# Performance work log

Hardware: AMD Instinct MI355X
Metric: run time of the kernel (lower is better)

## Reference

```python
import math
import jax, jax.numpy as jnp
import numpy as np

NUM_HEADS = 16
LN_EPS = 1e-5


def setup_inputs() -> dict:
    key = jax.random.key(0)
    ks = jax.random.split(key, 8)
    B, S, D = 2, 1024, 1024
    L, H = 4, NUM_HEADS
    hd = D // H
    return {
        "x": jax.random.normal(ks[0], (B, S, D), jnp.float32),
        "past_k": jax.random.normal(ks[1], (L, B, H, S, hd), jnp.float32),
        "past_v": jax.random.normal(ks[2], (L, B, H, S, hd), jnp.float32),
        "past_q": jax.random.normal(ks[3], (L, B, H, S, hd), jnp.float32),
        "Wqkv": jax.random.normal(ks[4], (3 * D, D), jnp.float32) * 0.02,
        "bqkv": jnp.zeros((3 * D,), jnp.float32),
        "Wout": jax.random.normal(ks[5], (D, D), jnp.float32) * 0.02,
        "bout": jnp.zeros((D,), jnp.float32),
    }


def reference(x, past_k, past_v, past_q, Wqkv, bqkv, Wout, bout):
    B, S, D = x.shape
    H = NUM_HEADS
    hd = D // H
    scale = 1.0 / math.sqrt(hd)

    # qkv projection + head split: [B,S,D] -> [B,H,S,hd] each
    qkv = x @ Wqkv.T + bqkv  # [B,S,3D]
    q, k, v = jnp.split(qkv, 3, axis=-1)
    split = lambda t: t.reshape(B, S, H, hd).transpose(0, 2, 1, 3)
    q, k, v = split(q), split(k), split(v)

    # causal token attention scores [B,H,S,S]
    token_scores = jnp.einsum("bhqd,bhkd->bhqk", q, k) * scale
    causal = jnp.triu(jnp.ones((S, S), bool), k=1)
    token_scores = jnp.where(causal, -jnp.inf, token_scores)

    # stack past layers: [L,B,H,S,hd] -> [B,S,L,D]
    def to_full(t):
        L = t.shape[0]
        return t.transpose(1, 3, 0, 2, 4).reshape(B, S, L, D)

    mem = jnp.concatenate([to_full(past_q), to_full(past_k), to_full(past_v)], axis=2)  # [B,S,M,D], M=3L
    M = mem.shape[2]

    # layer norm (no affine) over feature dim
    mu = mem.mean(-1, keepdims=True)
    var = mem.var(-1, keepdims=True)
    mem = (mem - mu) / jnp.sqrt(var + LN_EPS)

    # reproject through K/V slices of qkv weight
    Wk, bk = Wqkv[D:2 * D], bqkv[D:2 * D]
    Wv, bv = Wqkv[2 * D:], bqkv[2 * D:]
    rk = (mem @ Wk.T + bk).reshape(B, S, M, H, hd).transpose(0, 3, 1, 2, 4)  # [B,H,S,M,hd]
    rv = (mem @ Wv.T + bv).reshape(B, S, M, H, hd).transpose(0, 3, 1, 2, 4)

    # memory scores via per-position elementwise reduce [B,H,S,M]
    mem_scores = jnp.einsum("bhsd,bhsmd->bhsm", q, rk) * scale

    scores = jnp.concatenate([token_scores, mem_scores], axis=-1)  # [B,H,S,S+M]
    weights = jax.nn.softmax(scores, axis=-1)
    token_w, mem_w = weights[..., :S], weights[..., S:]

    token_ctx = jnp.einsum("bhqk,bhkd->bhqd", token_w, v)
    mem_ctx = jnp.einsum("bhsm,bhsmd->bhsd", mem_w, rv)
    attn = token_ctx + mem_ctx  # [B,H,S,hd]

    merged = attn.transpose(0, 2, 1, 3).reshape(B, S, D)
    out = merged @ Wout.T + bout
    return out, (k, v, q)
```

## Files before the change

kernel.cpp:

```cpp
#include <hip/hip_runtime.h>

#define BATCH 2
#define SEQ   1024
#define DIM   1024
#define NH    16
#define HD    64
#define NM    12
#define NTOK  (BATCH*SEQ)
#define MEMROWS (BATCH*SEQ*NM)
#define OUTT  2097152
#define NEGBIG (-1.0e30f)

typedef __attribute__((ext_vector_type(8))) short short8;
typedef __attribute__((ext_vector_type(4))) float f32x4;

__device__ __forceinline__ float bf2f(ushort u) {
    union { unsigned int i; float f; } t; t.i = ((unsigned int)u) << 16; return t.f;
}
__device__ __forceinline__ ushort f2bf(float f) {
    union { float f; unsigned int i; } t; t.f = f;
    unsigned int i = t.i;
    unsigned int lsb = (i >> 16) & 1u;
    i += 0x7fffu + lsb;
    return (ushort)(i >> 16);
}

__global__ __launch_bounds__(256) void cvt3_kernel(
    const float* __restrict__ a, ushort* __restrict__ ab, int na4,
    const float* __restrict__ b, ushort* __restrict__ bb, int nb4,
    const float* __restrict__ c, ushort* __restrict__ cb, int nc4)
{
    int i = blockIdx.x * 256 + threadIdx.x;
    if (i >= na4 + nb4 + nc4) return;
    const float* src; ushort* dst; int j;
    if (i < na4)            { src = a; dst = ab; j = i; }
    else if (i < na4 + nb4) { src = b; dst = bb; j = i - na4; }
    else                    { src = c; dst = cb; j = i - na4 - nb4; }
    float4 v = ((const float4*)src)[j];
    ushort4 o; o.x = f2bf(v.x); o.y = f2bf(v.y); o.z = f2bf(v.z); o.w = f2bf(v.w);
    ((ushort4*)dst)[j] = o;
}


#define QKV_BLKS 384
__global__ __launch_bounds__(256) void qkv_ln_fused_kernel(
    const ushort* __restrict__ xb, const ushort* __restrict__ Wb,
    const float* __restrict__ bias, float* __restrict__ out,
    ushort* __restrict__ qkvb,
    const float* __restrict__ pq, const float* __restrict__ pk,
    const float* __restrict__ pv, ushort* __restrict__ mem_n)
{
    const int bid = blockIdx.x;
    const int tid = threadIdx.x;
    if (bid < QKV_BLKS) {
        __shared__ ushort As[128][40];
        __shared__ ushort Bs[128][40];
        const int w = tid >> 6, lane = tid & 63;
        const int n = lane & 15, qd = lane >> 4;
        const int wr = (w >> 1) * 64, wc = (w & 1) * 64;
        const int row0 = (bid / 24) * 128, col0 = (bid % 24) * 128;
        const int r1 = tid >> 2, o1 = (tid & 3) * 8;
        const int r2 = (tid + 256) >> 2, o2 = ((tid + 256) & 3) * 8;

        f32x4 acc[4][4];
#pragma unroll
        for (int mt = 0; mt < 4; mt++)
#pragma unroll
            for (int nt = 0; nt < 4; nt++) acc[mt][nt] = (f32x4){0.f, 0.f, 0.f, 0.f};

        for (int k0 = 0; k0 < 1024; k0 += 32) {
            *(short8*)&As[r1][o1] = *(const short8*)(xb + (size_t)(row0 + r1) * 1024 + k0 + o1);
            *(short8*)&As[r2][o2] = *(const short8*)(xb + (size_t)(row0 + r2) * 1024 + k0 + o2);
            *(short8*)&Bs[r1][o1] = *(const short8*)(Wb + (size_t)(col0 + r1) * 1024 + k0 + o1);
            *(short8*)&Bs[r2][o2] = *(const short8*)(Wb + (size_t)(col0 + r2) * 1024 + k0 + o2);
            __syncthreads();
            short8 af[4], bf[4];
#pragma unroll
            for (int mt = 0; mt < 4; mt++) af[mt] = *(const short8*)&As[wr + mt * 16 + n][qd * 8];
#pragma unroll
            for (int nt = 0; nt < 4; nt++) bf[nt] = *(const short8*)&Bs[wc + nt * 16 + n][qd * 8];
#pragma unroll
            for (int mt = 0; mt < 4; mt++)
#pragma unroll
                for (int nt = 0; nt < 4; nt++)
                    acc[mt][nt] = __builtin_amdgcn_mfma_f32_16x16x32_bf16(af[mt], bf[nt], acc[mt][nt], 0, 0, 0);
            __syncthreads();
        }
#pragma unroll
        for (int mt = 0; mt < 4; mt++)
#pragma unroll
            for (int nt = 0; nt < 4; nt++)
#pragma unroll
                for (int r = 0; r < 4; r++) {
                    int row = row0 + wr + mt * 16 + qd * 4 + r;
                    int col = col0 + wc + nt * 16 + n;
                    float val = acc[mt][nt][r] + bias[col];
                    int t = col >> 10, h = (col >> 6) & 15, d = col & 63;
                    int b = row >> 10, s = row & 1023;
                    size_t idx = (((size_t)(b * NH + h) * SEQ + s) * HD) + d;
                    size_t base = (t == 0) ? (size_t)3 * OUTT : (t == 1) ? (size_t)OUTT : (size_t)2 * OUTT;
                    out[base + idx] = val;
                    qkvb[(size_t)t * OUTT + idx] = f2bf(val);
                }
    } else {
        const int wid = tid >> 6, lane = tid & 63;
        const int r = (bid - QKV_BLKS) * 4 + wid;
        const int idx = r % NM;
        const int bs = r / NM;
        const int s = bs & (SEQ - 1);
        const int b = bs >> 10;
        const int c = idx >> 2;
        const int l = idx & 3;
        const float* src = (c == 0) ? pq : ((c == 1) ? pk : pv);
        const size_t base = ((size_t)(l * BATCH + b) * NH) * (SEQ * HD) + (size_t)s * HD;

        float4 v4[4];
        float sum = 0.f, sumsq = 0.f;
#pragma unroll
        for (int p = 0; p < 4; p++) {
            int h = p * 4 + (lane >> 4);
            int d = (lane & 15) * 4;
            float4 v = *(const float4*)(src + base + (size_t)h * (SEQ * HD) + d);
            v4[p] = v;
            sum   += v.x + v.y + v.z + v.w;
            sumsq += v.x * v.x + v.y * v.y + v.z * v.z + v.w * v.w;
        }
#pragma unroll
        for (int off = 32; off > 0; off >>= 1) {
            sum   += __shfl_xor(sum, off);
            sumsq += __shfl_xor(sumsq, off);
        }
        float mu  = sum * (1.f / 1024.f);
        float var = fmaxf(sumsq * (1.f / 1024.f) - mu * mu, 0.f);
        float inv = rsqrtf(var + 1e-5f);
        ushort* dst = mem_n + (size_t)r * 1024;
#pragma unroll
        for (int p = 0; p < 4; p++) {
            int dp = (p * 64 + lane) * 4;
            ushort4 o;
            o.x = f2bf((v4[p].x - mu) * inv);
            o.y = f2bf((v4[p].y - mu) * inv);
            o.z = f2bf((v4[p].z - mu) * inv);
            o.w = f2bf((v4[p].w - mu) * inv);
            *(ushort4*)(dst + dp) = o;
        }
    }
}

__global__ __launch_bounds__(256) void mfma_out_kernel(
    const ushort* __restrict__ Ab, const ushort* __restrict__ Wb,
    const float* __restrict__ bias, float* __restrict__ C)
{
    __shared__ ushort As[128][40];
    __shared__ ushort Bs[128][40];
    const int tid = threadIdx.x;
    const int w = tid >> 6, lane = tid & 63;
    const int n = lane & 15, qd = lane >> 4;
    const int wr = (w >> 1) * 64, wc = (w & 1) * 64;
    const int row0 = blockIdx.y * 128, col0 = blockIdx.x * 128;
    const int r1 = tid >> 2, o1 = (tid & 3) * 8;
    const int r2 = (tid + 256) >> 2, o2 = ((tid + 256) & 3) * 8;

    f32x4 acc[4][4];
#pragma unroll
    for (int mt = 0; mt < 4; mt++)
#pragma unroll
        for (int nt = 0; nt < 4; nt++) acc[mt][nt] = (f32x4){0.f, 0.f, 0.f, 0.f};

    for (int k0 = 0; k0 < 1024; k0 += 32) {
        *(short8*)&As[r1][o1] = *(const short8*)(Ab + (size_t)(row0 + r1) * 1024 + k0 + o1);
        *(short8*)&As[r2][o2] = *(const short8*)(Ab + (size_t)(row0 + r2) * 1024 + k0 + o2);
        *(short8*)&Bs[r1][o1] = *(const short8*)(Wb + (size_t)(col0 + r1) * 1024 + k0 + o1);
        *(short8*)&Bs[r2][o2] = *(const short8*)(Wb + (size_t)(col0 + r2) * 1024 + k0 + o2);
        __syncthreads();
        short8 af[4], bf[4];
#pragma unroll
        for (int mt = 0; mt < 4; mt++) af[mt] = *(const short8*)&As[wr + mt * 16 + n][qd * 8];
#pragma unroll
        for (int nt = 0; nt < 4; nt++) bf[nt] = *(const short8*)&Bs[wc + nt * 16 + n][qd * 8];
#pragma unroll
        for (int mt = 0; mt < 4; mt++)
#pragma unroll
            for (int nt = 0; nt < 4; nt++)
                acc[mt][nt] = __builtin_amdgcn_mfma_f32_16x16x32_bf16(af[mt], bf[nt], acc[mt][nt], 0, 0, 0);
        __syncthreads();
    }
#pragma unroll
    for (int mt = 0; mt < 4; mt++)
#pragma unroll
        for (int nt = 0; nt < 4; nt++)
#pragma unroll
            for (int r = 0; r < 4; r++) {
                int row = row0 + wr + mt * 16 + qd * 4 + r;
                int col = col0 + wc + nt * 16 + n;
                C[(size_t)row * 1024 + col] = acc[mt][nt][r] + bias[col];
            }
}

__global__ __launch_bounds__(256) void mfma_vproj_kernel(
    const ushort* __restrict__ wvecb, const ushort* __restrict__ Wvb,
    const float* __restrict__ bv, const float* __restrict__ wmem,
    ushort* __restrict__ mergedb)
{
    __shared__ ushort As[128][40];
    __shared__ ushort Bs[64][40];
    const int tid = threadIdx.x;
    const int w = tid >> 6, lane = tid & 63;
    const int n = lane & 15, qd = lane >> 4;
    const int wr = (w >> 1) * 64, wc = (w & 1) * 32;
    const int row0 = blockIdx.x * 128;
    const int h = blockIdx.y;
    const int r1 = tid >> 2, o1 = (tid & 3) * 8;
    const int r2 = (tid + 256) >> 2, o2 = ((tid + 256) & 3) * 8;

    f32x4 acc[4][2];
#pragma unroll
    for (int mt = 0; mt < 4; mt++)
#pragma unroll
        for (int nt = 0; nt < 2; nt++) acc[mt][nt] = (f32x4){0.f, 0.f, 0.f, 0.f};

    for (int k0 = 0; k0 < 1024; k0 += 32) {
        *(short8*)&As[r1][o1] = *(const short8*)(wvecb + ((size_t)(row0 + r1) * NH + h) * 1024 + k0 + o1);
        *(short8*)&As[r2][o2] = *(const short8*)(wvecb + ((size_t)(row0 + r2) * NH + h) * 1024 + k0 + o2);
        *(short8*)&Bs[r1 & 63][o1] = *(const short8*)(Wvb + (size_t)(h * HD + (r1 & 63)) * 1024 + k0 + o1);
        __syncthreads();
        short8 af[4], bf[2];
#pragma unroll
        for (int mt = 0; mt < 4; mt++) af[mt] = *(const short8*)&As[wr + mt * 16 + n][qd * 8];
#pragma unroll
        for (int nt = 0; nt < 2; nt++) bf[nt] = *(const short8*)&Bs[wc + nt * 16 + n][qd * 8];
#pragma unroll
        for (int mt = 0; mt < 4; mt++)
#pragma unroll
            for (int nt = 0; nt < 2; nt++)
                acc[mt][nt] = __builtin_amdgcn_mfma_f32_16x16x32_bf16(af[mt], bf[nt], acc[mt][nt], 0, 0, 0);
        __syncthreads();
    }
#pragma unroll
    for (int mt = 0; mt < 4; mt++)
#pragma unroll
        for (int nt = 0; nt < 2; nt++)
#pragma unroll
            for (int r = 0; r < 4; r++) {
                int token = row0 + wr + mt * 16 + qd * 4 + r;
                int d = wc + nt * 16 + n;
                float ws = wmem[((size_t)token * NH + h) * 16 + 12];
                size_t mi = (size_t)token * DIM + h * HD + d;
                float val = bf2f(mergedb[mi]) + acc[mt][nt][r] + ws * bv[h * HD + d];
                mergedb[mi] = f2bf(val);
            }
}

#define MSC_T 8
__global__ __launch_bounds__(256) void msc_direct_kernel(
    const ushort* __restrict__ qkvb, const ushort* __restrict__ mem_n,
    const ushort* __restrict__ Wkb, const float* __restrict__ bqkv,
    float* __restrict__ msc0, float* __restrict__ msc1)
{
    __shared__ ushort wks[4][64][72];
    __shared__ ushort qpc[4][MSC_T][4][72];

    const int tid = threadIdx.x;
    const int w = tid >> 6, lane = tid & 63;
    const int n = lane & 15, qd = lane >> 4;
    const int t0 = blockIdx.x * MSC_T;
    const int kh = blockIdx.y;

    short8 af0[4], af1[4];
    {
        const int g = t0 + (n & 7), b = g >> 10, s = g & 1023;
#pragma unroll
        for (int hh = 0; hh < 4; hh++) {
            const int h = w * 4 + hh;
            const ushort* qrow = qkvb + (((size_t)(b * NH + h) * SEQ + s) * HD);
            af0[hh] = *(const short8*)(qrow + qd * 8);
            af1[hh] = *(const short8*)(qrow + 32 + qd * 8);
        }
    }
    float qbkv[4] = {0.f, 0.f, 0.f, 0.f};
    if (kh == 0) {
#pragma unroll
        for (int hh = 0; hh < 4; hh++) {
            const int h = w * 4 + hh;
            const float* bk = bqkv + DIM + h * HD;
            float s = 0.f;
#pragma unroll
            for (int j = 0; j < 8; j++) {
                s += bf2f((ushort)af0[hh][j]) * bk[qd * 8 + j];
                s += bf2f((ushort)af1[hh][j]) * bk[32 + qd * 8 + j];
            }
            s += __shfl_xor(s, 16);
            s += __shfl_xor(s, 32);
            qbkv[hh] = s;
        }
    }

    f32x4 acc[MSC_T];
#pragma unroll
    for (int t = 0; t < MSC_T; t++) acc[t] = (f32x4){0.f, 0.f, 0.f, 0.f};

    for (int ch = 0; ch < 8; ch++) {
        const int c0 = (kh * 8 + ch) * 64;
#pragma unroll
        for (int hh = 0; hh < 4; hh++) {
            const int h = w * 4 + hh;
            const ushort* wsrc = Wkb + (size_t)(h * HD + lane) * 1024 + c0;
#pragma unroll
            for (int j = 0; j < 4; j++) {
                ushort t16[16];
                *(short8*)&t16[0] = *(const short8*)(wsrc + j * 16);
                *(short8*)&t16[8] = *(const short8*)(wsrc + j * 16 + 8);
#pragma unroll
                for (int c = 0; c < 16; c++) wks[w][j * 16 + c][lane] = t16[c];
            }
#pragma unroll
            for (int nt = 0; nt < 4; nt++) {
                short8 bf0 = *(const short8*)&wks[w][nt * 16 + n][qd * 8];
                short8 bf1 = *(const short8*)&wks[w][nt * 16 + n][32 + qd * 8];
                f32x4 z = (f32x4){0.f, 0.f, 0.f, 0.f};
                z = __builtin_amdgcn_mfma_f32_16x16x32_bf16(af0[hh], bf0, z, 0, 0, 0);
                z = __builtin_amdgcn_mfma_f32_16x16x32_bf16(af1[hh], bf1, z, 0, 0, 0);
                if (qd < 2) {
#pragma unroll
                    for (int r = 0; r < 4; r++)
                        qpc[w][qd * 4 + r][hh][nt * 16 + n] = f2bf(z[r]);
                }
            }
        }
#pragma unroll
        for (int t = 0; t < MSC_T; t++) {
            const int g = t0 + t;
            const int mrow = (n < NM) ? n : 0;
            const ushort* mb = mem_n + ((size_t)g * NM + mrow) * 1024 + c0;
            short8 a0 = *(const short8*)&qpc[w][t][n & 3][qd * 8];
            short8 a1 = *(const short8*)&qpc[w][t][n & 3][32 + qd * 8];
            short8 b0 = *(const short8*)(mb + qd * 8);
            short8 b1 = *(const short8*)(mb + 32 + qd * 8);
            acc[t] = __builtin_amdgcn_mfma_f32_16x16x32_bf16(a0, b0, acc[t], 0, 0, 0);
            acc[t] = __builtin_amdgcn_mfma_f32_16x16x32_bf16(a1, b1, acc[t], 0, 0, 0);
        }
    }
#pragma unroll
    for (int t = 0; t < MSC_T; t++) {
        const size_t g = t0 + t;
#pragma unroll
        for (int r = 0; r < 4; r++) {
            float qb = __shfl(qbkv[r], t);
            if (qd == 0 && n < NM) {
                const int h = w * 4 + r;
                if (kh == 0)
                    msc0[(g * NH + h) * NM + n] = 0.125f * (acc[t][r] + qb);
                else
                    msc1[(g * NH + h) * NM + n] = 0.125f * acc[t][r];
            }
        }
    }
}

#define TQ 64
#define TK 64
__global__ __launch_bounds__(512) void flash_attn_kernel(
    const ushort* __restrict__ qkvb, const float* __restrict__ msc0,
    const float* __restrict__ msc1,
    ushort* __restrict__ mergedb, float* __restrict__ wmem)
{
    __shared__ __align__(16) char smem[55296];
    ushort (*Ks)[TK][72]  = (ushort (*)[TK][72])smem;
    ushort (*Vt)[HD][72]  = (ushort (*)[HD][72])(smem + 18432);
    ushort (*Ps)[16][72]  = (ushort (*)[16][72])(smem + 36864);
    float  (*cbuf)[64][25] = (float (*)[64][25])smem;

    const int bxr = blockIdx.x;
    const int qt = (bxr & 1) ? (bxr >> 1) : (15 - (bxr >> 1));
    const int bh = blockIdx.y;
    const int b = bh >> 4, h = bh & 15;
    const int tid = threadIdx.x;
    const int w = tid >> 6;
    const int g = w >> 2;
    const int wq = w & 3;
    const int lane = tid & 63;
    const int n = lane & 15;
    const int qd = lane >> 4;

    const ushort* qb = qkvb;
    const ushort* kb = qkvb + (size_t)OUTT;
    const ushort* vb = qkvb + (size_t)2 * OUTT;
    const size_t headoff = (size_t)bh * SEQ * HD;

    const int qrow0 = qt * TQ + wq * 16;
    const ushort* qp = qb + headoff + (size_t)(qrow0 + n) * HD;
    short8 qf0 = *(const short8*)(qp + qd * 8);
    short8 qf1 = *(const short8*)(qp + 32 + qd * 8);

    float mrow[4], lrow[4];
    f32x4 Oacc[4];
#pragma unroll
    for (int r = 0; r < 4; r++) { mrow[r] = NEGBIG; lrow[r] = 0.f; }
#pragma unroll
    for (int nt = 0; nt < 4; nt++) Oacc[nt] = (f32x4){0.f, 0.f, 0.f, 0.f};

    const int gtid = tid & 255;
    const int key = gtid >> 2;
    const int c0 = (gtid & 3) * 16;
    const int nsteps = (qt + 2) >> 1;

    for (int step = 0; step < nsteps; ++step) {
        const int kt = 2 * step + g;
        const bool act = (kt <= qt);
        if (act) {
            const ushort* kg = kb + headoff + (size_t)(kt * TK + key) * HD + c0;
            *(short8*)&Ks[g][key][c0]     = *(const short8*)kg;
            *(short8*)&Ks[g][key][c0 + 8] = *(const short8*)(kg + 8);
            const ushort* vg = vb + headoff + (size_t)(kt * TK + key) * HD + c0;
            ushort vs[16];
            *(short8*)&vs[0] = *(const short8*)vg;
            *(short8*)&vs[8] = *(const short8*)(vg + 8);
#pragma unroll
            for (int i = 0; i < 16; i++) Vt[g][c0 + i][key] = vs[i];
        }
        __syncthreads();
        if (act) {
            f32x4 sacc[4];
#pragma unroll
            for (int kc = 0; kc < 4; kc++) {
                short8 kf0 = *(const short8*)&Ks[g][kc * 16 + n][qd * 8];
                short8 kf1 = *(const short8*)&Ks[g][kc * 16 + n][32 + qd * 8];
                f32x4 z = (f32x4){0.f, 0.f, 0.f, 0.f};
                z = __builtin_amdgcn_mfma_f32_16x16x32_bf16(qf0, kf0, z, 0, 0, 0);
                z = __builtin_amdgcn_mfma_f32_16x16x32_bf16(qf1, kf1, z, 0, 0, 0);
                sacc[kc] = z;
            }
            const bool diag = (kt == qt);
#pragma unroll
            for (int kc = 0; kc < 4; kc++) {
#pragma unroll
                for (int r = 0; r < 4; r++) {
                    float sv = sacc[kc][r] * 0.125f;
                    if (diag) {
                        int qrow = qrow0 + qd * 4 + r;
                        int kk = kt * TK + kc * 16 + n;
                        if (kk > qrow) sv = NEGBIG;
                    }
                    sacc[kc][r] = sv;
                }
            }
            float alpha[4];
#pragma unroll
            for (int r = 0; r < 4; r++) {
                float mx = fmaxf(fmaxf(sacc[0][r], sacc[1][r]), fmaxf(sacc[2][r], sacc[3][r]));
                mx = fmaxf(mx, __shfl_xor(mx, 1));
                mx = fmaxf(mx, __shfl_xor(mx, 2));
                mx = fmaxf(mx, __shfl_xor(mx, 4));
                mx = fmaxf(mx, __shfl_xor(mx, 8));
                float mnew = fmaxf(mrow[r], mx);
                alpha[r] = __expf(mrow[r] - mnew);
                mrow[r] = mnew;
            }
            float psum[4] = {0.f, 0.f, 0.f, 0.f};
#pragma unroll
            for (int kc = 0; kc < 4; kc++) {
#pragma unroll
                for (int r = 0; r < 4; r++) {
                    float p = __expf(sacc[kc][r] - mrow[r]);
                    psum[r] += p;
                    Ps[w][qd * 4 + r][kc * 16 + n] = f2bf(p);
                }
            }
#pragma unroll
            for (int r = 0; r < 4; r++) {
                float ps = psum[r];
                ps += __shfl_xor(ps, 1);
                ps += __shfl_xor(ps, 2);
                ps += __shfl_xor(ps, 4);
                ps += __shfl_xor(ps, 8);
                lrow[r] = alpha[r] * lrow[r] + ps;
            }
#pragma unroll
            for (int nt = 0; nt < 4; nt++)
#pragma unroll
                for (int r = 0; r < 4; r++)
                    Oacc[nt][r] *= alpha[r];
            short8 pf0 = *(const short8*)&Ps[w][n][qd * 8];
            short8 pf1 = *(const short8*)&Ps[w][n][32 + qd * 8];
#pragma unroll
            for (int nt = 0; nt < 4; nt++) {
                short8 vf0 = *(const short8*)&Vt[g][nt * 16 + n][qd * 8];
                short8 vf1 = *(const short8*)&Vt[g][nt * 16 + n][32 + qd * 8];
                f32x4 z = Oacc[nt];
                z = __builtin_amdgcn_mfma_f32_16x16x32_bf16(pf0, vf0, z, 0, 0, 0);
                z = __builtin_amdgcn_mfma_f32_16x16x32_bf16(pf1, vf1, z, 0, 0, 0);
                Oacc[nt] = z;
            }
        }
        __syncthreads();
    }

    if (g == 1) {
        float* cb = cbuf[wq][lane];
#pragma unroll
        for (int nt = 0; nt < 4; nt++)
#pragma unroll
            for (int r = 0; r < 4; r++) cb[nt * 4 + r] = Oacc[nt][r];
#pragma unroll
        for (int r = 0; r < 4; r++) { cb[16 + r] = mrow[r]; cb[20 + r] = lrow[r]; }
    }
    __syncthreads();
    if (g == 1) return;

    {
        const float* cb = cbuf[wq][lane];
#pragma unroll
        for (int r = 0; r < 4; r++) {
            float m1 = cb[16 + r], l1 = cb[20 + r];
            float mnew = fmaxf(mrow[r], m1);
            float a0 = __expf(mrow[r] - mnew);
            float a1 = __expf(m1 - mnew);
            lrow[r] = a0 * lrow[r] + a1 * l1;
#pragma unroll
            for (int nt = 0; nt < 4; nt++)
                Oacc[nt][r] = a0 * Oacc[nt][r] + a1 * cb[nt * 4 + r];
            mrow[r] = mnew;
        }
    }

#pragma unroll
    for (int r = 0; r < 4; r++) {
        int srow = qrow0 + qd * 4 + r;
        const size_t midx = ((size_t)(b * SEQ + srow) * NH + h) * NM;
        float mpv[NM];
#pragma unroll
        for (int j = 0; j < NM; j++) mpv[j] = msc0[midx + j] + msc1[midx + j];
        float mm = NEGBIG;
#pragma unroll
        for (int j = 0; j < NM; j++) mm = fmaxf(mm, mpv[j]);
        float mf = fmaxf(mrow[r], mm);
        float al = __expf(mrow[r] - mf);
        float msum = 0.f;
#pragma unroll
        for (int j = 0; j < NM; j++) msum += __expf(mpv[j] - mf);
        float lf = al * lrow[r] + msum;
        float inv = 1.f / lf;
        float scale = al * inv;
        ushort* mrow_out = mergedb + (size_t)(b * SEQ + srow) * DIM + h * HD;
#pragma unroll
        for (int nt = 0; nt < 4; nt++)
            mrow_out[nt * 16 + n] = f2bf(Oacc[nt][r] * scale);
        size_t wb = ((size_t)(b * SEQ + srow) * NH + h) * 16;
        if (n < 12)       wmem[wb + n]  = __expf(mpv[n] - mf) * inv;
        else if (n == 12) wmem[wb + 12] = msum * inv;
    }
}

__global__ __launch_bounds__(256) void wvec_kernel(
    const float* __restrict__ wmem, const ushort* __restrict__ mem_n,
    ushort* __restrict__ wvecb)
{
    __shared__ ushort memL[NM][1032];
    __shared__ float wL[NH][NM];
    const int bs = blockIdx.x;
    const int tid = threadIdx.x;

    for (int t = tid; t < NM * 256; t += 256) {
        int m = t >> 8, c4 = (t & 255) << 2;
        *(ushort4*)&memL[m][c4] = *(const ushort4*)(mem_n + ((size_t)bs * NM + m) * 1024 + c4);
    }
    if (tid < NH * NM) {
        int h = tid / NM, m = tid % NM;
        wL[h][m] = wmem[((size_t)bs * NH + h) * 16 + m];
    }
    __syncthreads();

    for (int h = 0; h < NH; h++) {
#pragma unroll
        for (int c0 = 0; c0 < 1024; c0 += 256) {
            int c = c0 + tid;
            float acc = 0.f;
#pragma unroll
            for (int m = 0; m < NM; m++)
                acc = fmaf(wL[h][m], bf2f(memL[m][c]), acc);
            wvecb[((size_t)bs * NH + h) * 1024 + c] = f2bf(acc);
        }
    }
}

extern "C" void kernel_launch(void* const* d_in, const int* in_sizes, int n_in,
                              void* d_out, int out_size, void* d_ws, size_t ws_size,
                              hipStream_t stream) {
    const float* x    = (const float*)d_in[0];
    const float* pk   = (const float*)d_in[1];
    const float* pv   = (const float*)d_in[2];
    const float* pq   = (const float*)d_in[3];
    const float* Wqkv = (const float*)d_in[4];
    const float* bqkv = (const float*)d_in[5];
    const float* Wout = (const float*)d_in[6];
    const float* bout = (const float*)d_in[7];
    float* out = (float*)d_out;

    ushort* mem_n  = (ushort*)d_ws;
    ushort* wvecb  = mem_n + (size_t)MEMROWS * 1024;
    float*  msc    = (float*)(wvecb + (size_t)NTOK * NH * 1024);
    float*  wmem   = msc + (size_t)NTOK * NH * NM;
    ushort* qkvb   = (ushort*)(wmem + (size_t)NTOK * NH * 16);
    ushort* Wqkvb  = qkvb + (size_t)3 * OUTT;
    ushort* Woutb  = Wqkvb + (size_t)3072 * 1024;
    ushort* xb     = Woutb + (size_t)1024 * 1024;
    ushort* mergedb = xb;
    float*  msc2   = (float*)wvecb;

    const int na4 = NTOK * DIM / 4, nb4 = 3 * DIM * DIM / 4, nc4 = DIM * DIM / 4;

    cvt3_kernel<<<(na4 + nb4 + nc4 + 255) / 256, 256, 0, stream>>>(
        x, xb, na4, Wqkv, Wqkvb, nb4, Wout, Woutb, nc4);
    qkv_ln_fused_kernel<<<QKV_BLKS + MEMROWS / 4, 256, 0, stream>>>(
        xb, Wqkvb, bqkv, out, qkvb, pq, pk, pv, mem_n);
    msc_direct_kernel<<<dim3(NTOK / MSC_T, 2), 256, 0, stream>>>(
        qkvb, mem_n, Wqkvb + (size_t)DIM * DIM, bqkv, msc, msc2);
    flash_attn_kernel<<<dim3(16, 32), 512, 0, stream>>>(qkvb, msc, msc2, mergedb, wmem);
    wvec_kernel<<<NTOK, 256, 0, stream>>>(wmem, mem_n, wvecb);
    mfma_vproj_kernel<<<dim3(16, NH), 256, 0, stream>>>(
        wvecb, Wqkvb + (size_t)2 * DIM * DIM, bqkv + 2 * DIM, wmem, mergedb);
    mfma_out_kernel<<<dim3(8, 16), 256, 0, stream>>>(mergedb, Woutb, bout, out);
}
```

Before: 404.6 us.

## Pre-transpose Wk once and read B fragments directly in msc kernel

Adds a small kernel that transposes the bf16 Wk slice into a separate buffer. The memory-score kernel then loads MFMA B fragments straight from global memory instead of staging each chunk through LDS with a scalar transpose. The per-block token count is halved, which doubles the grid and uses only one quad of the 16-row MFMA output. This removes the LDS staging work and shrinks shared memory, but it adds a launch and makes each block read more of Wk from global memory.

```diff
diff --git a/kernel.cpp b/kernel.cpp
--- a/kernel.cpp
+++ b/kernel.cpp
@@ -39,6 +39,25 @@
     float4 v = ((const float4*)src)[j];
     ushort4 o; o.x = f2bf(v.x); o.y = f2bf(v.y); o.z = f2bf(v.z); o.w = f2bf(v.w);
     ((ushort4*)dst)[j] = o;
+}
+
+__global__ __launch_bounds__(256) void transpose_wk_kernel(
+    const ushort* __restrict__ Wkb, ushort* __restrict__ WkT)
+{
+    __shared__ ushort tile[64][72];
+    const int bx = (blockIdx.x & 15) * 64;
+    const int by = (blockIdx.x >> 4) * 64;
+    const int tid = threadIdx.x;
+    const int r = tid >> 2, c16 = (tid & 3) * 16;
+    *(short8*)&tile[r][c16]     = *(const short8*)(Wkb + (size_t)(by + r) * 1024 + bx + c16);
+    *(short8*)&tile[r][c16 + 8] = *(const short8*)(Wkb + (size_t)(by + r) * 1024 + bx + c16 + 8);
+    __syncthreads();
+    ushort tmp[16];
+#pragma unroll
+    for (int j = 0; j < 16; j++) tmp[j] = tile[c16 + j][r];
+    ushort* dst = WkT + (size_t)(bx + r) * 1024 + by + c16;
+    *(short8*)dst       = *(short8*)&tmp[0];
+    *(short8*)(dst + 8) = *(short8*)&tmp[8];
 }
 
 
@@ -251,13 +270,12 @@
             }
 }
 
-#define MSC_T 8
+#define MSC_T 4
 __global__ __launch_bounds__(256) void msc_direct_kernel(
     const ushort* __restrict__ qkvb, const ushort* __restrict__ mem_n,
-    const ushort* __restrict__ Wkb, const float* __restrict__ bqkv,
+    const ushort* __restrict__ WkT, const float* __restrict__ bqkv,
     float* __restrict__ msc0, float* __restrict__ msc1)
 {
-    __shared__ ushort wks[4][64][72];
     __shared__ ushort qpc[4][MSC_T][4][72];
 
     const int tid = threadIdx.x;
@@ -268,7 +286,7 @@
 
     short8 af0[4], af1[4];
     {
-        const int g = t0 + (n & 7), b = g >> 10, s = g & 1023;
+        const int g = t0 + (n & 3), b = g >> 10, s = g & 1023;
 #pragma unroll
         for (int hh = 0; hh < 4; hh++) {
             const int h = w * 4 + hh;
@@ -304,26 +322,18 @@
 #pragma unroll
         for (int hh = 0; hh < 4; hh++) {
             const int h = w * 4 + hh;
-            const ushort* wsrc = Wkb + (size_t)(h * HD + lane) * 1024 + c0;
-#pragma unroll
-            for (int j = 0; j < 4; j++) {
-                ushort t16[16];
-                *(short8*)&t16[0] = *(const short8*)(wsrc + j * 16);
-                *(short8*)&t16[8] = *(const short8*)(wsrc + j * 16 + 8);
-#pragma unroll
-                for (int c = 0; c < 16; c++) wks[w][j * 16 + c][lane] = t16[c];
-            }
 #pragma unroll
             for (int nt = 0; nt < 4; nt++) {
-                short8 bf0 = *(const short8*)&wks[w][nt * 16 + n][qd * 8];
-                short8 bf1 = *(const short8*)&wks[w][nt * 16 + n][32 + qd * 8];
+                const ushort* wt = WkT + (size_t)(c0 + nt * 16 + n) * 1024 + h * HD;
+                short8 bf0 = *(const short8*)(wt + qd * 8);
+                short8 bf1 = *(const short8*)(wt + 32 + qd * 8);
                 f32x4 z = (f32x4){0.f, 0.f, 0.f, 0.f};
                 z = __builtin_amdgcn_mfma_f32_16x16x32_bf16(af0[hh], bf0, z, 0, 0, 0);
                 z = __builtin_amdgcn_mfma_f32_16x16x32_bf16(af1[hh], bf1, z, 0, 0, 0);
-                if (qd < 2) {
+                if (qd == 0) {
 #pragma unroll
                     for (int r = 0; r < 4; r++)
-                        qpc[w][qd * 4 + r][hh][nt * 16 + n] = f2bf(z[r]);
+                        qpc[w][r][hh][nt * 16 + n] = f2bf(z[r]);
                 }
             }
         }
@@ -605,16 +615,18 @@
     ushort* Woutb  = Wqkvb + (size_t)3072 * 1024;
     ushort* xb     = Woutb + (size_t)1024 * 1024;
     ushort* mergedb = xb;
+    ushort* WkT    = xb + (size_t)NTOK * 1024;
     float*  msc2   = (float*)wvecb;
 
     const int na4 = NTOK * DIM / 4, nb4 = 3 * DIM * DIM / 4, nc4 = DIM * DIM / 4;
 
     cvt3_kernel<<<(na4 + nb4 + nc4 + 255) / 256, 256, 0, stream>>>(
         x, xb, na4, Wqkv, Wqkvb, nb4, Wout, Woutb, nc4);
+    transpose_wk_kernel<<<256, 256, 0, stream>>>(Wqkvb + (size_t)DIM * DIM, WkT);
     qkv_ln_fused_kernel<<<QKV_BLKS + MEMROWS / 4, 256, 0, stream>>>(
         xb, Wqkvb, bqkv, out, qkvb, pq, pk, pv, mem_n);
     msc_direct_kernel<<<dim3(NTOK / MSC_T, 2), 256, 0, stream>>>(
-        qkvb, mem_n, Wqkvb + (size_t)DIM * DIM, bqkv, msc, msc2);
+        qkvb, mem_n, WkT, bqkv, msc, msc2);
     flash_attn_kernel<<<dim3(16, 32), 512, 0, stream>>>(qkvb, msc, msc2, mergedb, wmem);
     wvec_kernel<<<NTOK, 256, 0, stream>>>(wmem, mem_n, wvecb);
     mfma_vproj_kernel<<<dim3(16, NH), 256, 0, stream>>>(
```

Result: slower. 452.0 us (+11.7%).
